# Kernel optimization log

Measured on AMD Instinct MI355X. Metric: run time of the kernel, lower is better.

Reference implementation:

```python
import jax, jax.numpy as jnp
import numpy as np

SMOOTH = 1e-05


def setup_inputs() -> dict:
    key = jax.random.key(0)
    k1, k2 = jax.random.split(key)
    N, C, H, W = 8, 4, 1024, 1024
    inp = jax.random.normal(k1, (N, C, H, W), dtype=jnp.float32)
    target = jax.random.randint(k2, (N, H, W), 0, C, dtype=jnp.int32)
    weights = jnp.ones((C,), dtype=jnp.float32)
    return {"input": inp, "target": target, "weights": weights}


def reference(input, target, weights):
    # softmax over class dim
    p = jax.nn.softmax(input, axis=1)            # [N, C, H, W]
    C = input.shape[1]
    onehot = jax.nn.one_hot(target, C, axis=1, dtype=p.dtype)  # [N, C, H, W]
    # per-sample, per-class dice over flattened spatial dims
    inter = jnp.sum(p * onehot, axis=(2, 3))      # [N, C]
    denom = jnp.sum(p, axis=(2, 3)) + jnp.sum(onehot, axis=(2, 3))  # [N, C]
    dice = (2.0 * inter + SMOOTH) / (denom + SMOOTH)  # [N, C]
    per_class_loss = 1.0 - jnp.mean(dice, axis=0)     # [C]
    total = jnp.sum(per_class_loss * weights)
    return total
```

## Files before the change

### kernel.cpp

```cpp
#include <hip/hip_runtime.h>


#define HWPIX (1024 * 1024)
#define NCLS 4
#define NSMP 8
#define GX 256
#define TPB 256
#define NVEC (HWPIX / 4)
#define ITERS 4
#define CHUNK (TPB * ITERS)
static constexpr float SMOOTH = 1e-5f;

__global__ __launch_bounds__(TPB) void dice_partial(
    const float* __restrict__ inp,
    const int* __restrict__ tgt,
    float* __restrict__ part)
{
    const int n = blockIdx.y;
    const float4* __restrict__ in4 = (const float4*)(inp + (size_t)n * NCLS * HWPIX);
    const int4* __restrict__ tg4 = (const int4*)(tgt + (size_t)n * HWPIX);

    const int base = blockIdx.x * CHUNK + threadIdx.x;

    float4 xa[ITERS], xb[ITERS], xc[ITERS], xd[ITERS];
    int4 tv[ITERS];
    #pragma unroll
    for (int s = 0; s < ITERS; ++s) {
        const int i = base + s * TPB;
        xa[s] = in4[i];
        xb[s] = in4[i + NVEC];
        xc[s] = in4[i + 2 * NVEC];
        xd[s] = in4[i + 3 * NVEC];
        tv[s] = tg4[i];
    }

    float i0 = 0.f, i1 = 0.f, i2 = 0.f, i3 = 0.f;
    float m0 = 0.f, m1 = 0.f, m2 = 0.f, m3 = 0.f;

    #pragma unroll
    for (int s = 0; s < ITERS; ++s) {
        float4 x0 = xa[s], x1 = xb[s], x2 = xc[s], x3 = xd[s];
        int4 t4 = tv[s];
        #pragma unroll
        for (int j = 0; j < 4; ++j) {
            float a = (j == 0) ? x0.x : (j == 1) ? x0.y : (j == 2) ? x0.z : x0.w;
            float b = (j == 0) ? x1.x : (j == 1) ? x1.y : (j == 2) ? x1.z : x1.w;
            float c = (j == 0) ? x2.x : (j == 1) ? x2.y : (j == 2) ? x2.z : x2.w;
            float d = (j == 0) ? x3.x : (j == 1) ? x3.y : (j == 2) ? x3.z : x3.w;
            int t   = (j == 0) ? t4.x : (j == 1) ? t4.y : (j == 2) ? t4.z : t4.w;

            float e0 = __expf(a);
            float e1 = __expf(b);
            float e2 = __expf(c);
            float e3 = __expf(d);
            float inv = __builtin_amdgcn_rcpf(e0 + e1 + e2 + e3);
            float p0 = e0 * inv, p1 = e1 * inv, p2 = e2 * inv, p3 = e3 * inv;

            i0 += (t == 0) ? p0 : 0.f;
            i1 += (t == 1) ? p1 : 0.f;
            i2 += (t == 2) ? p2 : 0.f;
            i3 += (t == 3) ? p3 : 0.f;
            m0 += p0 + ((t == 0) ? 1.f : 0.f);
            m1 += p1 + ((t == 1) ? 1.f : 0.f);
            m2 += p2 + ((t == 2) ? 1.f : 0.f);
            m3 += p3 + ((t == 3) ? 1.f : 0.f);
        }
    }

    float r[8] = {i0, i1, i2, i3, m0, m1, m2, m3};
    #pragma unroll
    for (int off = 32; off > 0; off >>= 1) {
        #pragma unroll
        for (int k = 0; k < 8; ++k) r[k] += __shfl_down(r[k], off);
    }

    __shared__ float sred[4][8];
    const int wave = threadIdx.x >> 6;
    const int lane = threadIdx.x & 63;
    if (lane == 0) {
        #pragma unroll
        for (int k = 0; k < 8; ++k) sred[wave][k] = r[k];
    }
    __syncthreads();
    if (threadIdx.x < 8) {
        float v = sred[0][threadIdx.x] + sred[1][threadIdx.x] +
                  sred[2][threadIdx.x] + sred[3][threadIdx.x];
        part[(threadIdx.x * NSMP + n) * GX + blockIdx.x] = v;
    }
}

__global__ __launch_bounds__(1024) void dice_final(
    const float* __restrict__ part,
    const float* __restrict__ w,
    float* __restrict__ out)
{
    __shared__ float sred[64];
    const int wave = threadIdx.x >> 6;
    const int lane = threadIdx.x & 63;

    #pragma unroll
    for (int q = 0; q < 4; ++q) {
        const int s = wave * 4 + q;
        const float* seg = part + s * GX;
        float v = seg[lane] + seg[lane + 64] + seg[lane + 128] + seg[lane + 192];
        #pragma unroll
        for (int off = 32; off > 0; off >>= 1) v += __shfl_down(v, off);
        if (lane == 0) sred[s] = v;
    }
    __syncthreads();

    if (threadIdx.x == 0) {
        float total = 0.f;
        #pragma unroll
        for (int c = 0; c < NCLS; ++c) {
            float dsum = 0.f;
            #pragma unroll
            for (int n = 0; n < NSMP; ++n) {
                float inter = sred[c * NSMP + n];
                float m     = sred[(4 + c) * NSMP + n];
                dsum += (2.f * inter + SMOOTH) / (m + SMOOTH);
            }
            total += w[c] * (1.f - dsum / (float)NSMP);
        }
        out[0] = total;
    }
}

extern "C" void kernel_launch(void* const* d_in, const int* in_sizes, int n_in,
                              void* d_out, int out_size, void* d_ws, size_t ws_size,
                              hipStream_t stream) {
    const float* inp = (const float*)d_in[0];
    const int* tgt   = (const int*)d_in[1];
    const float* w   = (const float*)d_in[2];
    float* out       = (float*)d_out;
    float* part      = (float*)d_ws;

    dim3 grid(GX, NSMP);
    dice_partial<<<grid, TPB, 0, stream>>>(inp, tgt, part);
    dice_final<<<1, 1024, 0, stream>>>(part, w, out);
}
```

Measured before the change: 35.25 us.

## Fuse final dice reduction into partial kernel via last-block atomic counter

Removes the separate single-block finalisation kernel. Each block of the partial kernel now bumps a global atomic counter, and the last block to finish reduces all partials (using float4 loads) and writes the loss. This aims to remove a kernel launch and the gap between the two kernels. In exchange it adds a memset of the counter before each launch and relies on release/acquire ordering for the partial stores made by the lanes other than thread 0.

```diff
diff --git a/kernel.cpp b/kernel.cpp
--- a/kernel.cpp
+++ b/kernel.cpp
@@ -9,12 +9,16 @@
 #define NVEC (HWPIX / 4)
 #define ITERS 4
 #define CHUNK (TPB * ITERS)
+#define NBLOCKS (GX * NSMP)
 static constexpr float SMOOTH = 1e-5f;
 
-__global__ __launch_bounds__(TPB) void dice_partial(
+__global__ __launch_bounds__(TPB) void dice_fused(
     const float* __restrict__ inp,
     const int* __restrict__ tgt,
-    float* __restrict__ part)
+    const float* __restrict__ w,
+    float* __restrict__ part,
+    unsigned int* __restrict__ counter,
+    float* __restrict__ out)
 {
     const int n = blockIdx.y;
     const float4* __restrict__ in4 = (const float4*)(inp + (size_t)n * NCLS * HWPIX);
@@ -87,25 +91,32 @@
                   sred[2][threadIdx.x] + sred[3][threadIdx.x];
         part[(threadIdx.x * NSMP + n) * GX + blockIdx.x] = v;
     }
-}
 
-__global__ __launch_bounds__(1024) void dice_final(
-    const float* __restrict__ part,
-    const float* __restrict__ w,
-    float* __restrict__ out)
-{
-    __shared__ float sred[64];
-    const int wave = threadIdx.x >> 6;
-    const int lane = threadIdx.x & 63;
+    __shared__ unsigned int amLast;
+    if (threadIdx.x == 0) {
+        unsigned int old = __hip_atomic_fetch_add(counter, 1u, __ATOMIC_RELEASE,
+                                                  __HIP_MEMORY_SCOPE_AGENT);
+        amLast = (old == NBLOCKS - 1) ? 1u : 0u;
+    }
+    __syncthreads();
+    if (!amLast) return;
 
+    if (threadIdx.x == 0) {
+        (void)__hip_atomic_load(counter, __ATOMIC_ACQUIRE,
+                                __HIP_MEMORY_SCOPE_AGENT);
+    }
+    __syncthreads();
+
+    __shared__ float s2[64];
     #pragma unroll
-    for (int q = 0; q < 4; ++q) {
-        const int s = wave * 4 + q;
-        const float* seg = part + s * GX;
-        float v = seg[lane] + seg[lane + 64] + seg[lane + 128] + seg[lane + 192];
+    for (int q = 0; q < 16; ++q) {
+        const int s = wave * 16 + q;
+        const float4* seg4 = (const float4*)(part + s * GX);
+        float4 v4 = seg4[lane];
+        float v = v4.x + v4.y + v4.z + v4.w;
         #pragma unroll
         for (int off = 32; off > 0; off >>= 1) v += __shfl_down(v, off);
-        if (lane == 0) sred[s] = v;
+        if (lane == 0) s2[s] = v;
     }
     __syncthreads();
 
@@ -115,9 +126,9 @@
         for (int c = 0; c < NCLS; ++c) {
             float dsum = 0.f;
             #pragma unroll
-            for (int n = 0; n < NSMP; ++n) {
-                float inter = sred[c * NSMP + n];
-                float m     = sred[(4 + c) * NSMP + n];
+            for (int nn = 0; nn < NSMP; ++nn) {
+                float inter = s2[c * NSMP + nn];
+                float m     = s2[(4 + c) * NSMP + nn];
                 dsum += (2.f * inter + SMOOTH) / (m + SMOOTH);
             }
             total += w[c] * (1.f - dsum / (float)NSMP);
@@ -134,8 +145,10 @@
     const float* w   = (const float*)d_in[2];
     float* out       = (float*)d_out;
     float* part      = (float*)d_ws;
+    unsigned int* counter = (unsigned int*)((char*)d_ws + 65536);
+
+    hipMemsetAsync(counter, 0, sizeof(unsigned int), stream);
 
     dim3 grid(GX, NSMP);
-    dice_partial<<<grid, TPB, 0, stream>>>(inp, tgt, part);
-    dice_final<<<1, 1024, 0, stream>>>(part, w, out);
+    dice_fused<<<grid, TPB, 0, stream>>>(inp, tgt, w, part, counter, out);
 }
```

After: 100.2 us. 2.84x slower.
